# Optimization experiments

Measured on AMD Instinct MI355X. Metric: run time of the kernel, lower is better.

Reference implementation:

```python
import jax, jax.numpy as jnp
import numpy as np

N_WORD, N_DOC, E = 20000, 20000, 500000
H, O, D = 4, 32, 128  # heads, out per head, hidden*heads
NEG_SLOPE = 0.2


def setup_inputs() -> dict:
    key = jax.random.key(0)
    ks = jax.random.split(key, 24)
    rn = lambda k, s, sc=0.1: jax.random.normal(k, s, dtype=jnp.float32) * sc
    ri = lambda k, s, hi: jax.random.randint(k, s, 0, hi, dtype=jnp.int32)
    return {
        'x_word': rn(ks[0], (N_WORD, 300), 1.0),
        'x_doc': rn(ks[1], (N_DOC, D), 1.0),
        'Wp_word': rn(ks[2], (300, D)), 'bp_word': jnp.zeros((D,), jnp.float32),
        'Wp_doc': rn(ks[3], (D, D)), 'bp_doc': jnp.zeros((D,), jnp.float32),
        'Wsrc': rn(ks[4], (2, 3, D, D)), 'bsrc': jnp.zeros((2, 3, D), jnp.float32),
        'Wdst': rn(ks[5], (2, 3, D, D)), 'bdst': jnp.zeros((2, 3, D), jnp.float32),
        'attn': rn(ks[6], (2, 3, H, O)), 'bconv': jnp.zeros((2, 3, D), jnp.float32),
        'Wc1': rn(ks[7], (D, 64)), 'bc1': jnp.zeros((64,), jnp.float32),
        'Wc2': rn(ks[8], (64, 64)), 'bc2': jnp.zeros((64,), jnp.float32),
        'src_wd': ri(ks[9], (E,), N_WORD), 'dst_wd': ri(ks[10], (E,), N_DOC),
        'src_dw': ri(ks[11], (E,), N_DOC), 'dst_dw': ri(ks[12], (E,), N_WORD),
        'src_dd': ri(ks[13], (E,), N_DOC), 'dst_dd': ri(ks[14], (E,), N_DOC),
    }


def _gatv2(h_src, h_dst, src, dst, Ws, bs, Wd, bd, a, bias, n_dst):
    # GATv2Conv (DGL): e = a . leaky_relu(Ws h_u + Wd h_v); edge softmax per dst; sum alpha*Ws h_u
    fs = (h_src @ Ws + bs).reshape(-1, H, O)           # [N_src,H,O]
    fd = (h_dst @ Wd + bd).reshape(-1, H, O)           # [N_dst,H,O]
    e = jax.nn.leaky_relu(fs[src] + fd[dst], NEG_SLOPE)  # [E,H,O]
    score = jnp.einsum('eho,ho->eh', e, a)             # [E,H]
    m = jax.lax.stop_gradient(jax.ops.segment_max(score, dst, num_segments=n_dst))
    ex = jnp.exp(score - m[dst])
    s = jax.ops.segment_sum(ex, dst, num_segments=n_dst)
    alpha = ex / s[dst]                                 # per-dst softmax
    rst = jax.ops.segment_sum(alpha[:, :, None] * fs[src], dst, num_segments=n_dst)
    return rst + bias.reshape(1, H, O)


def reference(x_word, x_doc, Wp_word, bp_word, Wp_doc, bp_doc, Wsrc, bsrc, Wdst, bdst,
              attn, bconv, Wc1, bc1, Wc2, bc2, src_wd, dst_wd, src_dw, dst_dw, src_dd, dst_dd):
    h_w = x_word @ Wp_word + bp_word
    h_d = x_doc @ Wp_doc + bp_doc
    for l in range(2):
        o_wd = _gatv2(h_w, h_d, src_wd, dst_wd, Wsrc[l, 0], bsrc[l, 0], Wdst[l, 0], bdst[l, 0], attn[l, 0], bconv[l, 0], N_DOC)
        o_dw = _gatv2(h_d, h_w, src_dw, dst_dw, Wsrc[l, 1], bsrc[l, 1], Wdst[l, 1], bdst[l, 1], attn[l, 1], bconv[l, 1], N_WORD)
        o_dd = _gatv2(h_d, h_d, src_dd, dst_dd, Wsrc[l, 2], bsrc[l, 2], Wdst[l, 2], bdst[l, 2], attn[l, 2], bconv[l, 2], N_DOC)
        h_d = ((o_wd + o_dd) * 0.5).reshape(N_DOC, D)   # mean over 2 relations into 'document'
        h_w = o_dw.reshape(N_WORD, D)                    # mean over 1 relation into 'word'
    z = jax.nn.relu(h_d @ Wc1 + bc1)
    return z @ Wc2 + bc2  # [N_DOC, len_label]
```

## Files before the change

### kernel.cpp

```cpp
#include <hip/hip_runtime.h>

#define NNODE 20000
#define NEDGE 500000
#define CAP 64
#define RCHUNK 2048
#define NRANGE 8
#define RSZ 2500
#define SCAP 70000
#define XW 64

typedef __attribute__((ext_vector_type(8))) short bf16x8;
typedef __attribute__((ext_vector_type(8))) unsigned short u16x8;
typedef __attribute__((ext_vector_type(4))) float f32x4;

__device__ __forceinline__ unsigned short f2bf(float f) {
    unsigned u = __float_as_uint(f);
    return (unsigned short)((u + 0x7FFFu + ((u >> 16) & 1u)) >> 16);
}
__device__ __forceinline__ float bf2f(unsigned short h) {
    return __uint_as_float((unsigned)h << 16);
}

__device__ __forceinline__ void split_one(
    const float* __restrict__ B, unsigned short* __restrict__ Bt,
    int K, int N, int Kp, int i)
{
    int n = i / Kp, k = i % Kp;
    float v = (k < K) ? B[(size_t)k * N + n] : 0.f;
    unsigned short h = f2bf(v);
    Bt[i] = h;
    Bt[(size_t)N * Kp + i] = f2bf(v - bf2f(h));
}

__device__ __forceinline__ void split_row4(
    const float* __restrict__ X, unsigned short* __restrict__ A2,
    int K, int Kp, int r, int c)
{
    float v[4];
#pragma unroll
    for (int j = 0; j < 4; ++j) v[j] = (c + j < K) ? X[(size_t)r * K + c + j] : 0.f;
    ushort4 hi, lo;
    unsigned short h;
    h = f2bf(v[0]); hi.x = h; lo.x = f2bf(v[0] - bf2f(h));
    h = f2bf(v[1]); hi.y = h; lo.y = f2bf(v[1] - bf2f(h));
    h = f2bf(v[2]); hi.z = h; lo.z = f2bf(v[2] - bf2f(h));
    h = f2bf(v[3]); hi.w = h; lo.w = f2bf(v[3] - bf2f(h));
    *reinterpret_cast<ushort4*>(A2 + (size_t)r * 2 * Kp + c) = hi;
    *reinterpret_cast<ushort4*>(A2 + (size_t)r * 2 * Kp + Kp + c) = lo;
}

__global__ __launch_bounds__(256) void prep_all_kernel(
    const float* __restrict__ Wp_word, const float* __restrict__ Wp_doc,
    const float* __restrict__ Wsrc, const float* __restrict__ Wdst,
    const float* __restrict__ Wc1, const float* __restrict__ Wc2,
    const float* __restrict__ xw, const float* __restrict__ xd,
    unsigned short* __restrict__ WtPw, unsigned short* __restrict__ WtPd,
    unsigned short* __restrict__ WtCat,
    unsigned short* __restrict__ WtC1, unsigned short* __restrict__ WtC2,
    unsigned short* __restrict__ Ax, unsigned short* __restrict__ Axd)
{
    int i = blockIdx.x * 256 + threadIdx.x;
    const int S0 = 128 * 320, S1 = 128 * 128, S2 = 6 * 256 * 128;
    const int S3 = 64 * 128, S4 = 64 * 64;
    const int X1 = NNODE * 80, X2 = NNODE * 32;
    if (i < S0) { split_one(Wp_word, WtPw, 300, 128, 320, i); return; }
    i -= S0;
    if (i < S1) { split_one(Wp_doc, WtPd, 128, 128, 128, i); return; }
    i -= S1;
    if (i < S2) {
        int lc = i / (256 * 128), rem = i % (256 * 128);
        int n = rem / 128, k = rem % 128;
        int l = lc / 3, c = lc % 3;
        int half = n >> 7, nn = n & 127;
        const float* M;
        if (c == 0)      M = half ? (Wdst + (size_t)(l * 3 + 1) * 16384) : (Wsrc + (size_t)(l * 3 + 0) * 16384);
        else if (c == 1) M = half ? (Wsrc + (size_t)(l * 3 + 1) * 16384) : (Wdst + (size_t)(l * 3 + 0) * 16384);
        else             M = half ? (Wdst + (size_t)(l * 3 + 2) * 16384) : (Wsrc + (size_t)(l * 3 + 2) * 16384);
        float v = M[(size_t)k * 128 + nn];
        unsigned short h = f2bf(v);
        unsigned short* Bt = WtCat + (size_t)lc * 65536;
        Bt[(size_t)n * 128 + k] = h;
        Bt[32768 + (size_t)n * 128 + k] = f2bf(v - bf2f(h));
        return;
    }
    i -= S2;
    if (i < S3) { split_one(Wc1, WtC1, 128, 64, 128, i); return; }
    i -= S3;
    if (i < S4) { split_one(Wc2, WtC2, 64, 64, 64, i); return; }
    i -= S4;
    if (i < X1) {
        int r = i / 80, c = (i % 80) * 4;
        split_row4(xw, Ax, 300, 320, r, c);
        return;
    }
    i -= X1;
    if (i < X2) {
        int r = i / 32, c = (i % 32) * 4;
        split_row4(xd, Axd, 128, 128, r, c);
    }
}

template<int BM, int BN, int MODE>
__global__ __launch_bounds__(512) void gemm_mfma_kernel(
    const unsigned short* __restrict__ A2,
    const unsigned short* __restrict__ Bt,
    const float* __restrict__ b0,
    float* __restrict__ C0, unsigned short* __restrict__ S0,
    int M, int Kp, int do_relu)
{
    constexpr int FM = BM / 32;
    constexpr int FN = BN / 64;
    __shared__ unsigned short As[2][BM][40];
    __shared__ unsigned short Bs[2][BN][40];
    const int tid = threadIdx.x;
    const int m0 = blockIdx.x * BM;
    const int wid = tid >> 6, lane = tid & 63;
    const int wm = wid >> 2, wn = wid & 3;
    const int lr = lane & 15, kg = lane >> 4;

    f32x4 acc[FM][FN] = {};
    const size_t KA = 2 * (size_t)Kp;
    const size_t PB = (size_t)BN * Kp;

    for (int k0 = 0; k0 < Kp; k0 += 32) {
#pragma unroll
        for (int idx = tid; idx < BM * 4; idx += 512) {
            int row = idx >> 2, ck = idx & 3;
            u16x8 hi = {0,0,0,0,0,0,0,0}, lo = {0,0,0,0,0,0,0,0};
            if (m0 + row < M) {
                const unsigned short* ap = A2 + (size_t)(m0 + row) * KA + k0 + ck * 8;
                hi = *reinterpret_cast<const u16x8*>(ap);
                lo = *reinterpret_cast<const u16x8*>(ap + Kp);
            }
            *reinterpret_cast<u16x8*>(&As[0][row][ck * 8]) = hi;
            *reinterpret_cast<u16x8*>(&As[1][row][ck * 8]) = lo;
        }
#pragma unroll
        for (int idx = tid; idx < BN * 4; idx += 512) {
            int nr = idx >> 2, ck = idx & 3;
            const unsigned short* bp = Bt + (size_t)nr * Kp + k0 + ck * 8;
            *reinterpret_cast<u16x8*>(&Bs[0][nr][ck * 8]) = *reinterpret_cast<const u16x8*>(bp);
            *reinterpret_cast<u16x8*>(&Bs[1][nr][ck * 8]) = *reinterpret_cast<const u16x8*>(bp + PB);
        }
        __syncthreads();
        bf16x8 ah[FM], al[FM], bh[FN], bl[FN];
#pragma unroll
        for (int fm = 0; fm < FM; ++fm) {
            ah[fm] = *reinterpret_cast<const bf16x8*>(&As[0][wm * (BM / 2) + fm * 16 + lr][kg * 8]);
            al[fm] = *reinterpret_cast<const bf16x8*>(&As[1][wm * (BM / 2) + fm * 16 + lr][kg * 8]);
        }
#pragma unroll
        for (int fn = 0; fn < FN; ++fn) {
            bh[fn] = *reinterpret_cast<const bf16x8*>(&Bs[0][wn * (BN / 4) + fn * 16 + lr][kg * 8]);
            bl[fn] = *reinterpret_cast<const bf16x8*>(&Bs[1][wn * (BN / 4) + fn * 16 + lr][kg * 8]);
        }
#pragma unroll
        for (int fm = 0; fm < FM; ++fm)
#pragma unroll
            for (int fn = 0; fn < FN; ++fn) {
                acc[fm][fn] = __builtin_amdgcn_mfma_f32_16x16x32_bf16(ah[fm], bh[fn], acc[fm][fn], 0, 0, 0);
                acc[fm][fn] = __builtin_amdgcn_mfma_f32_16x16x32_bf16(al[fm], bh[fn], acc[fm][fn], 0, 0, 0);
                acc[fm][fn] = __builtin_amdgcn_mfma_f32_16x16x32_bf16(ah[fm], bl[fn], acc[fm][fn], 0, 0, 0);
            }
        __syncthreads();
    }
#pragma unroll
    for (int fm = 0; fm < FM; ++fm)
#pragma unroll
        for (int fn = 0; fn < FN; ++fn) {
            int gc = wn * (BN / 4) + fn * 16 + lr;
            float bv = b0[gc];
#pragma unroll
            for (int j = 0; j < 4; ++j) {
                int gr = m0 + wm * (BM / 2) + fm * 16 + kg * 4 + j;
                if (gr < M) {
                    float v = acc[fm][fn][j] + bv;
                    if (do_relu) v = fmaxf(v, 0.f);
                    if (MODE == 0) {
                        C0[(size_t)gr * BN + gc] = v;
                    } else {
                        unsigned short h = f2bf(v);
                        S0[(size_t)gr * 2 * BN + gc] = h;
                        S0[(size_t)gr * 2 * BN + BN + gc] = f2bf(v - bf2f(h));
                    }
                }
            }
        }
}

struct Cat3Args {
    const unsigned short* A[3];
    const unsigned short* Bt[3];
    const float* bs0[3];
    const float* bs1[3];
    unsigned short* P0[3];
    unsigned short* P1[3];
};

__global__ __launch_bounds__(512) void gemm_cat3_kernel(Cat3Args args, int M)
{
    constexpr int BM = 128, BN = 256, FM = 4, FN = 4, Kp = 128;
    const int y = blockIdx.y;
    const unsigned short* __restrict__ A2 = args.A[y];
    const unsigned short* __restrict__ Bt = args.Bt[y];
    __shared__ unsigned short As[2][BM][40];
    __shared__ unsigned short Bs[2][BN][40];
    const int tid = threadIdx.x;
    const int m0 = blockIdx.x * BM;
    const int wid = tid >> 6, lane = tid & 63;
    const int wm = wid >> 2, wn = wid & 3;
    const int lr = lane & 15, kg = lane >> 4;

    f32x4 acc[FM][FN] = {};
    const size_t KA = 2 * (size_t)Kp;
    const size_t PB = (size_t)BN * Kp;

    for (int k0 = 0; k0 < Kp; k0 += 32) {
#pragma unroll
        for (int idx = tid; idx < BM * 4; idx += 512) {
            int row = idx >> 2, ck = idx & 3;
            u16x8 hi = {0,0,0,0,0,0,0,0}, lo = {0,0,0,0,0,0,0,0};
            if (m0 + row < M) {
                const unsigned short* ap = A2 + (size_t)(m0 + row) * KA + k0 + ck * 8;
                hi = *reinterpret_cast<const u16x8*>(ap);
                lo = *reinterpret_cast<const u16x8*>(ap + Kp);
            }
            *reinterpret_cast<u16x8*>(&As[0][row][ck * 8]) = hi;
            *reinterpret_cast<u16x8*>(&As[1][row][ck * 8]) = lo;
        }
#pragma unroll
        for (int idx = tid; idx < BN * 4; idx += 512) {
            int nr = idx >> 2, ck = idx & 3;
            const unsigned short* bp = Bt + (size_t)nr * Kp + k0 + ck * 8;
            *reinterpret_cast<u16x8*>(&Bs[0][nr][ck * 8]) = *reinterpret_cast<const u16x8*>(bp);
            *reinterpret_cast<u16x8*>(&Bs[1][nr][ck * 8]) = *reinterpret_cast<const u16x8*>(bp + PB);
        }
        __syncthreads();
        bf16x8 ah[FM], al[FM], bh[FN], bl[FN];
#pragma unroll
        for (int fm = 0; fm < FM; ++fm) {
            ah[fm] = *reinterpret_cast<const bf16x8*>(&As[0][wm * 64 + fm * 16 + lr][kg * 8]);
            al[fm] = *reinterpret_cast<const bf16x8*>(&As[1][wm * 64 + fm * 16 + lr][kg * 8]);
        }
#pragma unroll
        for (int fn = 0; fn < FN; ++fn) {
            bh[fn] = *reinterpret_cast<const bf16x8*>(&Bs[0][wn * 64 + fn * 16 + lr][kg * 8]);
            bl[fn] = *reinterpret_cast<const bf16x8*>(&Bs[1][wn * 64 + fn * 16 + lr][kg * 8]);
        }
#pragma unroll
        for (int fm = 0; fm < FM; ++fm)
#pragma unroll
            for (int fn = 0; fn < FN; ++fn) {
                acc[fm][fn] = __builtin_amdgcn_mfma_f32_16x16x32_bf16(ah[fm], bh[fn], acc[fm][fn], 0, 0, 0);
                acc[fm][fn] = __builtin_amdgcn_mfma_f32_16x16x32_bf16(al[fm], bh[fn], acc[fm][fn], 0, 0, 0);
                acc[fm][fn] = __builtin_amdgcn_mfma_f32_16x16x32_bf16(ah[fm], bl[fn], acc[fm][fn], 0, 0, 0);
            }
        __syncthreads();
    }
    const float* __restrict__ bs0 = args.bs0[y];
    const float* __restrict__ bs1 = args.bs1[y];
    unsigned short* __restrict__ P0 = args.P0[y];
    unsigned short* __restrict__ P1 = args.P1[y];
#pragma unroll
    for (int fm = 0; fm < FM; ++fm)
#pragma unroll
        for (int fn = 0; fn < FN; ++fn) {
            int gc = wn * 64 + fn * 16 + lr;
            float bv = (gc < 128) ? bs0[gc] : bs1[gc - 128];
#pragma unroll
            for (int j = 0; j < 4; ++j) {
                int gr = m0 + wm * 64 + fm * 16 + kg * 4 + j;
                if (gr < M) {
                    float v = acc[fm][fn][j] + bv;
                    unsigned short h = f2bf(v);
                    if (gc < 128) P0[(size_t)gr * 128 + gc] = h;
                    else          P1[(size_t)gr * 128 + gc - 128] = h;
                }
            }
        }
}

__global__ __launch_bounds__(256) void route_kernel(
    const int* __restrict__ s0, const int* __restrict__ d0,
    const int* __restrict__ s1, const int* __restrict__ d1,
    const int* __restrict__ s2, const int* __restrict__ d2,
    unsigned* __restrict__ stage, int* __restrict__ scur)
{
    __shared__ unsigned sbuf[RCHUNK];
    __shared__ int hcnt[NRANGE], hoff[NRANGE], gbase[NRANGE], hcur[NRANGE];
    const int rel = blockIdx.y;
    const int c0 = blockIdx.x * RCHUNK;
    const int n = (c0 + RCHUNK <= NEDGE) ? RCHUNK : (NEDGE - c0);
    const int tid = threadIdx.x;
    const int* sp = rel == 0 ? s0 : rel == 1 ? s1 : s2;
    const int* dp = rel == 0 ? d0 : rel == 1 ? d1 : d2;

    if (tid < NRANGE) hcnt[tid] = 0;
    __syncthreads();
    for (int i = tid; i < n; i += 256) atomicAdd(&hcnt[dp[c0 + i] / RSZ], 1);
    __syncthreads();
    if (tid == 0) {
        int o = 0;
        for (int r = 0; r < NRANGE; ++r) {
            hoff[r] = o; hcur[r] = o; o += hcnt[r];
            gbase[r] = atomicAdd(&scur[rel * NRANGE + r], hcnt[r]);
        }
    }
    __syncthreads();
    for (int i = tid; i < n; i += 256) {
        int d = dp[c0 + i], s = sp[c0 + i];
        int k = atomicAdd(&hcur[d / RSZ], 1);
        sbuf[k] = ((unsigned)d << 16) | (unsigned)s;
    }
    __syncthreads();
    for (int r = 0; r < NRANGE; ++r) {
        int cnt = hcnt[r];
        int lim = SCAP - gbase[r];
        if (cnt > lim) cnt = lim;
        unsigned* dst = stage + (size_t)(rel * NRANGE + r) * SCAP + gbase[r];
        for (int i = tid; i < cnt; i += 256) dst[i] = sbuf[hoff[r] + i];
    }
}

__global__ __launch_bounds__(256) void xfill_kernel(
    const unsigned* __restrict__ stage, const int* __restrict__ scur,
    int* __restrict__ deg, unsigned short* __restrict__ csr)
{
    const int r = blockIdx.x & 7;
    const int w = blockIdx.x >> 3;
    const int tid = threadIdx.x;
#pragma unroll
    for (int rel = 0; rel < 3; ++rel) {
        int total = scur[rel * NRANGE + r];
        if (total > SCAP) total = SCAP;
        const unsigned* st = stage + (size_t)(rel * NRANGE + r) * SCAP;
        int* dg = deg + rel * NNODE;
        unsigned short* cb = csr + (size_t)rel * NNODE * CAP;
        for (int i = w * 256 + tid; i < total; i += XW * 256) {
            unsigned p = st[i];
            int d = (int)(p >> 16), s = (int)(p & 0xFFFFu);
            int k = atomicAdd(&dg[d], 1);
            if (k < CAP) cb[(size_t)d * CAP + k] = (unsigned short)s;
        }
    }
}

__device__ __forceinline__ void rel_raw(
    const unsigned short* __restrict__ fsP,
    const unsigned short* __restrict__ fdP,
    const unsigned short* __restrict__ csrc,
    const float* __restrict__ attnRow,
    int d, int lane, int iBeg, int iEnd,
    float& ssum, float* __restrict__ acc)
{
    float fdv[8], av[8];
    {
        u16x8 t = *reinterpret_cast<const u16x8*>(fdP + (size_t)d * 128 + lane * 8);
#pragma unroll
        for (int j = 0; j < 8; ++j) fdv[j] = bf2f(t[j]);
    }
#pragma unroll
    for (int j = 0; j < 8; ++j) av[j] = attnRow[lane * 8 + j];

    int i = iBeg;
    for (; i + 4 <= iEnd; i += 4) {
        int s0 = csrc[i], s1 = csrc[i + 1], s2 = csrc[i + 2], s3 = csrc[i + 3];
        u16x8 q0 = *reinterpret_cast<const u16x8*>(fsP + (size_t)s0 * 128 + lane * 8);
        u16x8 q1 = *reinterpret_cast<const u16x8*>(fsP + (size_t)s1 * 128 + lane * 8);
        u16x8 q2 = *reinterpret_cast<const u16x8*>(fsP + (size_t)s2 * 128 + lane * 8);
        u16x8 q3 = *reinterpret_cast<const u16x8*>(fsP + (size_t)s3 * 128 + lane * 8);
        float u0[8], u1[8], u2[8], u3[8];
        float pa0 = 0.f, pb0 = 0.f, pa1 = 0.f, pb1 = 0.f;
        float pa2 = 0.f, pb2 = 0.f, pa3 = 0.f, pb3 = 0.f;
#pragma unroll
        for (int j = 0; j < 8; ++j) {
            u0[j] = bf2f(q0[j]); float z = u0[j] + fdv[j];
            pa0 = fmaf(av[j], z, pa0); pb0 = fmaf(av[j], fabsf(z), pb0);
        }
#pragma unroll
        for (int j = 0; j < 8; ++j) {
            u1[j] = bf2f(q1[j]); float z = u1[j] + fdv[j];
            pa1 = fmaf(av[j], z, pa1); pb1 = fmaf(av[j], fabsf(z), pb1);
        }
#pragma unroll
        for (int j = 0; j < 8; ++j) {
            u2[j] = bf2f(q2[j]); float z = u2[j] + fdv[j];
            pa2 = fmaf(av[j], z, pa2); pb2 = fmaf(av[j], fabsf(z), pb2);
        }
#pragma unroll
        for (int j = 0; j < 8; ++j) {
            u3[j] = bf2f(q3[j]); float z = u3[j] + fdv[j];
            pa3 = fmaf(av[j], z, pa3); pb3 = fmaf(av[j], fabsf(z), pb3);
        }
        float p0 = fmaf(0.4f, pb0, 0.6f * pa0);
        float p1 = fmaf(0.4f, pb1, 0.6f * pa1);
        float p2 = fmaf(0.4f, pb2, 0.6f * pa2);
        float p3 = fmaf(0.4f, pb3, 0.6f * pa3);
        p0 += __shfl_xor(p0, 1); p0 += __shfl_xor(p0, 2);
        p1 += __shfl_xor(p1, 1); p1 += __shfl_xor(p1, 2);
        p2 += __shfl_xor(p2, 1); p2 += __shfl_xor(p2, 2);
        p3 += __shfl_xor(p3, 1); p3 += __shfl_xor(p3, 2);
        float w0 = __expf(p0), w1 = __expf(p1);
        float w2 = __expf(p2), w3 = __expf(p3);
        ssum += (w0 + w1) + (w2 + w3);
#pragma unroll
        for (int j = 0; j < 8; ++j)
            acc[j] += fmaf(w0, u0[j], w1 * u1[j]) + fmaf(w2, u2[j], w3 * u3[j]);
    }
    for (; i < iEnd; ++i) {
        int s0 = csrc[i];
        u16x8 q0 = *reinterpret_cast<const u16x8*>(fsP + (size_t)s0 * 128 + lane * 8);
        float u0[8];
        float pa = 0.f, pb = 0.f;
#pragma unroll
        for (int j = 0; j < 8; ++j) {
            u0[j] = bf2f(q0[j]); float z = u0[j] + fdv[j];
            pa = fmaf(av[j], z, pa); pb = fmaf(av[j], fabsf(z), pb);
        }
        float p0 = fmaf(0.4f, pb, 0.6f * pa);
        p0 += __shfl_xor(p0, 1); p0 += __shfl_xor(p0, 2);
        float w = __expf(p0);
        ssum += w;
#pragma unroll
        for (int j = 0; j < 8; ++j) acc[j] = fmaf(w, u0[j], acc[j]);
    }
}

struct ConvJob {
    const unsigned short *fsA, *fdA;
    const int* degA; const unsigned short* csrA;
    const float *attnA, *biasA;
    const unsigned short *fsB, *fdB;
    const int* degB; const unsigned short* csrB;
    const float *attnB, *biasB;
    float wscale;
    unsigned short* sp;
};

__global__ __launch_bounds__(256) void gat_conv3_kernel(
    ConvJob J0, ConvJob J1, int nblk0)
{
    const bool first = ((int)blockIdx.x < nblk0);
    const ConvJob J = first ? J0 : J1;
    const int b = first ? (int)blockIdx.x : (int)blockIdx.x - nblk0;
    int gid = b * 256 + threadIdx.x;
    int d = gid >> 5;
    int lane = gid & 15;
    int half = (gid >> 4) & 1;
    if (d >= NNODE) return;

    float ssum = 0.f;
    float acc[8];
#pragma unroll
    for (int j = 0; j < 8; ++j) acc[j] = 0.f;
    float r[8];

    if (J.fsB) {
        const unsigned short* fs = half ? J.fsB : J.fsA;
        const unsigned short* fd = half ? J.fdB : J.fdA;
        const int* dgp           = half ? J.degB : J.degA;
        const unsigned short* cs = half ? J.csrB : J.csrA;
        const float* at          = half ? J.attnB : J.attnA;
        int deg = dgp[d]; if (deg > CAP) deg = CAP;
        rel_raw(fs, fd, cs, at, d, lane, d * CAP, d * CAP + deg, ssum, acc);
        float inv = (ssum > 0.f) ? J.wscale / ssum : 0.f;
#pragma unroll
        for (int j = 0; j < 8; ++j) {
            r[j] = inv * acc[j];
            r[j] += __shfl_xor(r[j], 16);
        }
    } else {
        int deg = J.degA[d]; if (deg > CAP) deg = CAP;
        int h = (deg + 1) >> 1;
        int iB = d * CAP + (half ? h : 0);
        int iE = d * CAP + (half ? deg : h);
        rel_raw(J.fsA, J.fdA, J.csrA, J.attnA, d, lane, iB, iE, ssum, acc);
        ssum += __shfl_xor(ssum, 16);
#pragma unroll
        for (int j = 0; j < 8; ++j) acc[j] += __shfl_xor(acc[j], 16);
        float inv = (ssum > 0.f) ? J.wscale / ssum : 0.f;
#pragma unroll
        for (int j = 0; j < 8; ++j) r[j] = inv * acc[j];
    }

    if (half == 0) {
        u16x8 hv, lv;
#pragma unroll
        for (int j = 0; j < 8; ++j) {
            float bb = J.biasA[lane * 8 + j];
            if (J.biasB) bb += J.biasB[lane * 8 + j];
            float o = J.wscale * bb + r[j];
            unsigned short hh = f2bf(o);
            hv[j] = hh;
            lv[j] = f2bf(o - bf2f(hh));
        }
        *reinterpret_cast<u16x8*>(J.sp + (size_t)d * 256 + lane * 8) = hv;
        *reinterpret_cast<u16x8*>(J.sp + (size_t)d * 256 + 128 + lane * 8) = lv;
    }
}

extern "C" void kernel_launch(void* const* d_in, const int* in_sizes, int n_in,
                              void* d_out, int out_size, void* d_ws, size_t ws_size,
                              hipStream_t stream)
{
    const float* x_word  = (const float*)d_in[0];
    const float* x_doc   = (const float*)d_in[1];
    const float* Wp_word = (const float*)d_in[2];
    const float* bp_word = (const float*)d_in[3];
    const float* Wp_doc  = (const float*)d_in[4];
    const float* bp_doc  = (const float*)d_in[5];
    const float* Wsrc    = (const float*)d_in[6];
    const float* bsrc    = (const float*)d_in[7];
    const float* Wdst    = (const float*)d_in[8];
    const float* bdst    = (const float*)d_in[9];
    const float* attn    = (const float*)d_in[10];
    const float* bconv   = (const float*)d_in[11];
    const float* Wc1     = (const float*)d_in[12];
    const float* bc1     = (const float*)d_in[13];
    const float* Wc2     = (const float*)d_in[14];
    const float* bc2     = (const float*)d_in[15];
    const int* src_wd = (const int*)d_in[16];
    const int* dst_wd = (const int*)d_in[17];
    const int* src_dw = (const int*)d_in[18];
    const int* dst_dw = (const int*)d_in[19];
    const int* src_dd = (const int*)d_in[20];
    const int* dst_dd = (const int*)d_in[21];

    const size_t NP = (size_t)NNODE * 128;
    unsigned short* U = (unsigned short*)d_ws;
    unsigned short* Pfs_wd = U;
    unsigned short* Pfd_dw = U + 1 * NP;
    unsigned short* Pfd_wd = U + 2 * NP;
    unsigned short* Pfs_dw = U + 3 * NP;
    unsigned short* Pfs_dd = U + 4 * NP;
    unsigned short* Pfd_dd = U + 5 * NP;
    unsigned short* AswA = U + 6 * NP;
    unsigned short* AsdA = AswA + 2 * NP;
    unsigned short* AswB = AsdA + 2 * NP;
    unsigned short* AsdB = AswB + 2 * NP;
    unsigned short* WtPw  = AsdB + 2 * NP;
    unsigned short* WtPd  = WtPw + 81920;
    unsigned short* WtCat = WtPd + 32768;
    unsigned short* WtC1  = WtCat + 393216;
    unsigned short* WtC2  = WtC1 + 16384;
    unsigned short* Ax  = Pfs_wd;
    unsigned short* Axd = AswB;
    unsigned short* Az  = AswB;
    int* I    = (int*)(WtC2 + 8192);
    int* deg  = I;
    int* scur = I + 3 * NNODE;
    unsigned* stage = (unsigned*)(scur + 32);
    unsigned short* csrp = (unsigned short*)(stage + 3 * NRANGE * SCAP);

    const int GB128 = (NNODE + 127) / 128;
    const int CB32 = (NNODE * 32) / 256;
    const int RB = (NEDGE + RCHUNK - 1) / RCHUNK;

    (void)hipMemsetAsync(deg, 0, (3 * NNODE + 32) * sizeof(int), stream);
    route_kernel<<<dim3(RB, 3), 256, 0, stream>>>(
        src_wd, dst_wd, src_dw, dst_dw, src_dd, dst_dd, stage, scur);
    xfill_kernel<<<NRANGE * XW, 256, 0, stream>>>(stage, scur, deg, csrp);

    const int PREP = 266240 + NNODE * 112;
    prep_all_kernel<<<(PREP + 255) / 256, 256, 0, stream>>>(
        Wp_word, Wp_doc, Wsrc, Wdst, Wc1, Wc2, x_word, x_doc,
        WtPw, WtPd, WtCat, WtC1, WtC2, Ax, Axd);

    gemm_mfma_kernel<128, 128, 2><<<GB128, 512, 0, stream>>>(
        Ax, WtPw, bp_word, nullptr, AswA, NNODE, 320, 0);
    gemm_mfma_kernel<128, 128, 2><<<GB128, 512, 0, stream>>>(
        Axd, WtPd, bp_doc, nullptr, AsdA, NNODE, 128, 0);

    const unsigned short* Asw_in = AswA;
    const unsigned short* Asd_in = AsdA;
    for (int l = 0; l < 2; ++l) {
        const int l3 = l * 3;
        Cat3Args ca;
        ca.A[0] = Asw_in; ca.A[1] = Asd_in; ca.A[2] = Asd_in;
        ca.Bt[0] = WtCat + (size_t)(l3 + 0) * 65536;
        ca.Bt[1] = WtCat + (size_t)(l3 + 1) * 65536;
        ca.Bt[2] = WtCat + (size_t)(l3 + 2) * 65536;
        ca.bs0[0] = bsrc + (l3 + 0) * 128; ca.bs1[0] = bdst + (l3 + 1) * 128;
        ca.bs0[1] = bdst + (l3 + 0) * 128; ca.bs1[1] = bsrc + (l3 + 1) * 128;
        ca.bs0[2] = bsrc + (l3 + 2) * 128; ca.bs1[2] = bdst + (l3 + 2) * 128;
        ca.P0[0] = Pfs_wd; ca.P1[0] = Pfd_dw;
        ca.P0[1] = Pfd_wd; ca.P1[1] = Pfs_dw;
        ca.P0[2] = Pfs_dd; ca.P1[2] = Pfd_dd;
        gemm_cat3_kernel<<<dim3(GB128, 3), 512, 0, stream>>>(ca, NNODE);

        ConvJob jd;
        jd.fsA = Pfs_wd; jd.fdA = Pfd_wd; jd.degA = deg;             jd.csrA = csrp;
        jd.attnA = attn + (l3 + 0) * 128; jd.biasA = bconv + (l3 + 0) * 128;
        jd.fsB = Pfs_dd; jd.fdB = Pfd_dd; jd.degB = deg + 2 * NNODE; jd.csrB = csrp + (size_t)2 * NNODE * CAP;
        jd.attnB = attn + (l3 + 2) * 128; jd.biasB = bconv + (l3 + 2) * 128;
        jd.wscale = 0.5f; jd.sp = (l == 0 ? AsdB : AsdA);

        if (l == 0) {
            ConvJob jw;
            jw.fsA = Pfs_dw; jw.fdA = Pfd_dw; jw.degA = deg + NNODE; jw.csrA = csrp + (size_t)NNODE * CAP;
            jw.attnA = attn + (l3 + 1) * 128; jw.biasA = bconv + (l3 + 1) * 128;
            jw.fsB = nullptr; jw.fdB = nullptr; jw.degB = nullptr; jw.csrB = nullptr;
            jw.attnB = nullptr; jw.biasB = nullptr;
            jw.wscale = 1.0f; jw.sp = AswB;
            gat_conv3_kernel<<<2 * CB32, 256, 0, stream>>>(jd, jw, CB32);
        } else {
            gat_conv3_kernel<<<CB32, 256, 0, stream>>>(jd, jd, CB32);
        }
        Asw_in = AswB;
        Asd_in = AsdB;
    }

    gemm_mfma_kernel<128, 64, 2><<<GB128, 512, 0, stream>>>(
        AsdA, WtC1, bc1, nullptr, Az, NNODE, 128, 1);
    gemm_mfma_kernel<128, 64, 0><<<GB128, 512, 0, stream>>>(
        Az, WtC2, bc2, (float*)d_out, nullptr, NNODE, 64, 0);
}
```

Measured before the change: 370.6 us.

## Fuse routing with weight prep, batch projection GEMMs, widen GAT conv to 64 lanes per node

Merges the edge-routing kernel into the weight/input split kernel as extra blocks, and launches both input projection GEMMs in one grid via a shared gemm body. The GAT aggregation kernel now assigns 64 threads per destination node instead of 32, splitting each node's edge list into two or four segments and combining them with extra cross-lane shuffles. The goal is fewer launches and more parallelism per high-degree node. The cost is more shuffle reductions and shared-memory use in the fused prep kernel.

```diff
diff --git a/kernel.cpp b/kernel.cpp
--- a/kernel.cpp
+++ b/kernel.cpp
@@ -49,7 +49,13 @@
     *reinterpret_cast<ushort4*>(A2 + (size_t)r * 2 * Kp + Kp + c) = lo;
 }
 
-__global__ __launch_bounds__(256) void prep_all_kernel(
+#define RB_ROUTE ((NEDGE + RCHUNK - 1) / RCHUNK)
+
+__global__ __launch_bounds__(256) void build_prep_kernel(
+    const int* __restrict__ s0, const int* __restrict__ d0,
+    const int* __restrict__ s1, const int* __restrict__ d1,
+    const int* __restrict__ s2, const int* __restrict__ d2,
+    unsigned* __restrict__ stage, int* __restrict__ scur,
     const float* __restrict__ Wp_word, const float* __restrict__ Wp_doc,
     const float* __restrict__ Wsrc, const float* __restrict__ Wdst,
     const float* __restrict__ Wc1, const float* __restrict__ Wc2,
@@ -59,7 +65,44 @@
     unsigned short* __restrict__ WtC1, unsigned short* __restrict__ WtC2,
     unsigned short* __restrict__ Ax, unsigned short* __restrict__ Axd)
 {
-    int i = blockIdx.x * 256 + threadIdx.x;
+    __shared__ unsigned sbuf[RCHUNK];
+    __shared__ int hcnt[NRANGE], hoff[NRANGE], gbase[NRANGE], hcur[NRANGE];
+    const int tid = threadIdx.x;
+    if ((int)blockIdx.x < 3 * RB_ROUTE) {
+        const int rel = blockIdx.x / RB_ROUTE;
+        const int c0 = (blockIdx.x % RB_ROUTE) * RCHUNK;
+        const int n = (c0 + RCHUNK <= NEDGE) ? RCHUNK : (NEDGE - c0);
+        const int* sp = rel == 0 ? s0 : rel == 1 ? s1 : s2;
+        const int* dp = rel == 0 ? d0 : rel == 1 ? d1 : d2;
+
+        if (tid < NRANGE) hcnt[tid] = 0;
+        __syncthreads();
+        for (int i = tid; i < n; i += 256) atomicAdd(&hcnt[dp[c0 + i] / RSZ], 1);
+        __syncthreads();
+        if (tid == 0) {
+            int o = 0;
+            for (int r = 0; r < NRANGE; ++r) {
+                hoff[r] = o; hcur[r] = o; o += hcnt[r];
+                gbase[r] = atomicAdd(&scur[rel * NRANGE + r], hcnt[r]);
+            }
+        }
+        __syncthreads();
+        for (int i = tid; i < n; i += 256) {
+            int d = dp[c0 + i], s = sp[c0 + i];
+            int k = atomicAdd(&hcur[d / RSZ], 1);
+            sbuf[k] = ((unsigned)d << 16) | (unsigned)s;
+        }
+        __syncthreads();
+        for (int r = 0; r < NRANGE; ++r) {
+            int cnt = hcnt[r];
+            int lim = SCAP - gbase[r];
+            if (cnt > lim) cnt = lim;
+            unsigned* dst = stage + (size_t)(rel * NRANGE + r) * SCAP + gbase[r];
+            for (int i = tid; i < cnt; i += 256) dst[i] = sbuf[hoff[r] + i];
+        }
+        return;
+    }
+    int i = ((int)blockIdx.x - 3 * RB_ROUTE) * 256 + tid;
     const int S0 = 128 * 320, S1 = 128 * 128, S2 = 6 * 256 * 128;
     const int S3 = 64 * 128, S4 = 64 * 64;
     const int X1 = NNODE * 80, X2 = NNODE * 32;
@@ -100,20 +143,41 @@
     }
 }
 
+__global__ __launch_bounds__(256) void xfill_kernel(
+    const unsigned* __restrict__ stage, const int* __restrict__ scur,
+    int* __restrict__ deg, unsigned short* __restrict__ csr)
+{
+    const int r = blockIdx.x & 7;
+    const int w = blockIdx.x >> 3;
+    const int tid = threadIdx.x;
+#pragma unroll
+    for (int rel = 0; rel < 3; ++rel) {
+        int total = scur[rel * NRANGE + r];
+        if (total > SCAP) total = SCAP;
+        const unsigned* st = stage + (size_t)(rel * NRANGE + r) * SCAP;
+        int* dg = deg + rel * NNODE;
+        unsigned short* cb = csr + (size_t)rel * NNODE * CAP;
+        for (int i = w * 256 + tid; i < total; i += XW * 256) {
+            unsigned p = st[i];
+            int d = (int)(p >> 16), s = (int)(p & 0xFFFFu);
+            int k = atomicAdd(&dg[d], 1);
+            if (k < CAP) cb[(size_t)d * CAP + k] = (unsigned short)s;
+        }
+    }
+}
+
 template<int BM, int BN, int MODE>
-__global__ __launch_bounds__(512) void gemm_mfma_kernel(
+__device__ __forceinline__ void gemm_body(
     const unsigned short* __restrict__ A2,
     const unsigned short* __restrict__ Bt,
     const float* __restrict__ b0,
     float* __restrict__ C0, unsigned short* __restrict__ S0,
-    int M, int Kp, int do_relu)
+    int M, int Kp, int do_relu, int m0,
+    unsigned short (*As)[BM][40], unsigned short (*Bs)[BN][40])
 {
     constexpr int FM = BM / 32;
     constexpr int FN = BN / 64;
-    __shared__ unsigned short As[2][BM][40];
-    __shared__ unsigned short Bs[2][BN][40];
     const int tid = threadIdx.x;
-    const int m0 = blockIdx.x * BM;
     const int wid = tid >> 6, lane = tid & 63;
     const int wm = wid >> 2, wn = wid & 3;
     const int lr = lane & 15, kg = lane >> 4;
@@ -188,6 +252,37 @@
         }
 }
 
+template<int BM, int BN, int MODE>
+__global__ __launch_bounds__(512) void gemm_mfma_kernel(
+    const unsigned short* __restrict__ A2,
+    const unsigned short* __restrict__ Bt,
+    const float* __restrict__ b0,
+    float* __restrict__ C0, unsigned short* __restrict__ S0,
+    int M, int Kp, int do_relu)
+{
+    __shared__ unsigned short As[2][BM][40];
+    __shared__ unsigned short Bs[2][BN][40];
+    gemm_body<BM, BN, MODE>(A2, Bt, b0, C0, S0, M, Kp, do_relu,
+                            blockIdx.x * BM, As, Bs);
+}
+
+struct Proj2Args {
+    const unsigned short* A[2];
+    const unsigned short* Bt[2];
+    const float* b0[2];
+    unsigned short* S0[2];
+    int Kp[2];
+};
+
+__global__ __launch_bounds__(512) void gemm_proj2_kernel(Proj2Args a, int M)
+{
+    __shared__ unsigned short As[2][128][40];
+    __shared__ unsigned short Bs[2][128][40];
+    const int y = blockIdx.y;
+    gemm_body<128, 128, 2>(a.A[y], a.Bt[y], a.b0[y], nullptr, a.S0[y],
+                           M, a.Kp[y], 0, blockIdx.x * 128, As, Bs);
+}
+
 struct Cat3Args {
     const unsigned short* A[3];
     const unsigned short* Bt[3];
@@ -280,71 +375,6 @@
         }
 }
 
-__global__ __launch_bounds__(256) void route_kernel(
-    const int* __restrict__ s0, const int* __restrict__ d0,
-    const int* __restrict__ s1, const int* __restrict__ d1,
-    const int* __restrict__ s2, const int* __restrict__ d2,
-    unsigned* __restrict__ stage, int* __restrict__ scur)
-{
-    __shared__ unsigned sbuf[RCHUNK];
-    __shared__ int hcnt[NRANGE], hoff[NRANGE], gbase[NRANGE], hcur[NRANGE];
-    const int rel = blockIdx.y;
-    const int c0 = blockIdx.x * RCHUNK;
-    const int n = (c0 + RCHUNK <= NEDGE) ? RCHUNK : (NEDGE - c0);
-    const int tid = threadIdx.x;
-    const int* sp = rel == 0 ? s0 : rel == 1 ? s1 : s2;
-    const int* dp = rel == 0 ? d0 : rel == 1 ? d1 : d2;
-
-    if (tid < NRANGE) hcnt[tid] = 0;
-    __syncthreads();
-    for (int i = tid; i < n; i += 256) atomicAdd(&hcnt[dp[c0 + i] / RSZ], 1);
-    __syncthreads();
-    if (tid == 0) {
-        int o = 0;
-        for (int r = 0; r < NRANGE; ++r) {
-            hoff[r] = o; hcur[r] = o; o += hcnt[r];
-            gbase[r] = atomicAdd(&scur[rel * NRANGE + r], hcnt[r]);
-        }
-    }
-    __syncthreads();
-    for (int i = tid; i < n; i += 256) {
-        int d = dp[c0 + i], s = sp[c0 + i];
-        int k = atomicAdd(&hcur[d / RSZ], 1);
-        sbuf[k] = ((unsigned)d << 16) | (unsigned)s;
-    }
-    __syncthreads();
-    for (int r = 0; r < NRANGE; ++r) {
-        int cnt = hcnt[r];
-        int lim = SCAP - gbase[r];
-        if (cnt > lim) cnt = lim;
-        unsigned* dst = stage + (size_t)(rel * NRANGE + r) * SCAP + gbase[r];
-        for (int i = tid; i < cnt; i += 256) dst[i] = sbuf[hoff[r] + i];
-    }
-}
-
-__global__ __launch_bounds__(256) void xfill_kernel(
-    const unsigned* __restrict__ stage, const int* __restrict__ scur,
-    int* __restrict__ deg, unsigned short* __restrict__ csr)
-{
-    const int r = blockIdx.x & 7;
-    const int w = blockIdx.x >> 3;
-    const int tid = threadIdx.x;
-#pragma unroll
-    for (int rel = 0; rel < 3; ++rel) {
-        int total = scur[rel * NRANGE + r];
-        if (total > SCAP) total = SCAP;
-        const unsigned* st = stage + (size_t)(rel * NRANGE + r) * SCAP;
-        int* dg = deg + rel * NNODE;
-        unsigned short* cb = csr + (size_t)rel * NNODE * CAP;
-        for (int i = w * 256 + tid; i < total; i += XW * 256) {
-            unsigned p = st[i];
-            int d = (int)(p >> 16), s = (int)(p & 0xFFFFu);
-            int k = atomicAdd(&dg[d], 1);
-            if (k < CAP) cb[(size_t)d * CAP + k] = (unsigned short)s;
-        }
-    }
-}
-
 __device__ __forceinline__ void rel_raw(
     const unsigned short* __restrict__ fsP,
     const unsigned short* __restrict__ fdP,
@@ -437,16 +467,16 @@
     unsigned short* sp;
 };
 
-__global__ __launch_bounds__(256) void gat_conv3_kernel(
+__global__ __launch_bounds__(256) void gat_conv4_kernel(
     ConvJob J0, ConvJob J1, int nblk0)
 {
     const bool first = ((int)blockIdx.x < nblk0);
     const ConvJob J = first ? J0 : J1;
     const int b = first ? (int)blockIdx.x : (int)blockIdx.x - nblk0;
-    int gid = b * 256 + threadIdx.x;
-    int d = gid >> 5;
-    int lane = gid & 15;
-    int half = (gid >> 4) & 1;
+    const int tid = threadIdx.x;
+    const int d = b * 4 + (tid >> 6);
+    const int lane = tid & 15;
+    const int group = (tid >> 4) & 3;
     if (d >= NNODE) return;
 
     float ssum = 0.f;
@@ -456,34 +486,44 @@
     float r[8];
 
     if (J.fsB) {
-        const unsigned short* fs = half ? J.fsB : J.fsA;
-        const unsigned short* fd = half ? J.fdB : J.fdA;
-        const int* dgp           = half ? J.degB : J.degA;
-        const unsigned short* cs = half ? J.csrB : J.csrA;
-        const float* at          = half ? J.attnB : J.attnA;
+        const int rel = group >> 1, hf = group & 1;
+        const unsigned short* fs = rel ? J.fsB : J.fsA;
+        const unsigned short* fd = rel ? J.fdB : J.fdA;
+        const int* dgp           = rel ? J.degB : J.degA;
+        const unsigned short* cs = rel ? J.csrB : J.csrA;
+        const float* at          = rel ? J.attnB : J.attnA;
         int deg = dgp[d]; if (deg > CAP) deg = CAP;
-        rel_raw(fs, fd, cs, at, d, lane, d * CAP, d * CAP + deg, ssum, acc);
+        int h0 = (deg + 1) >> 1;
+        int iB = d * CAP + (hf ? h0 : 0);
+        int iE = d * CAP + (hf ? deg : h0);
+        rel_raw(fs, fd, cs, at, d, lane, iB, iE, ssum, acc);
+        ssum += __shfl_xor(ssum, 16);
+#pragma unroll
+        for (int j = 0; j < 8; ++j) acc[j] += __shfl_xor(acc[j], 16);
         float inv = (ssum > 0.f) ? J.wscale / ssum : 0.f;
 #pragma unroll
         for (int j = 0; j < 8; ++j) {
             r[j] = inv * acc[j];
-            r[j] += __shfl_xor(r[j], 16);
+            r[j] += __shfl_xor(r[j], 32);
         }
     } else {
         int deg = J.degA[d]; if (deg > CAP) deg = CAP;
-        int h = (deg + 1) >> 1;
-        int iB = d * CAP + (half ? h : 0);
-        int iE = d * CAP + (half ? deg : h);
+        int iB = d * CAP + ((deg * group) >> 2);
+        int iE = d * CAP + ((deg * (group + 1)) >> 2);
         rel_raw(J.fsA, J.fdA, J.csrA, J.attnA, d, lane, iB, iE, ssum, acc);
         ssum += __shfl_xor(ssum, 16);
-#pragma unroll
-        for (int j = 0; j < 8; ++j) acc[j] += __shfl_xor(acc[j], 16);
+        ssum += __shfl_xor(ssum, 32);
+#pragma unroll
+        for (int j = 0; j < 8; ++j) {
+            acc[j] += __shfl_xor(acc[j], 16);
+            acc[j] += __shfl_xor(acc[j], 32);
+        }
         float inv = (ssum > 0.f) ? J.wscale / ssum : 0.f;
 #pragma unroll
         for (int j = 0; j < 8; ++j) r[j] = inv * acc[j];
     }
 
-    if (half == 0) {
+    if (group == 0) {
         u16x8 hv, lv;
 #pragma unroll
         for (int j = 0; j < 8; ++j) {
@@ -553,23 +593,21 @@
     unsigned short* csrp = (unsigned short*)(stage + 3 * NRANGE * SCAP);
 
     const int GB128 = (NNODE + 127) / 128;
-    const int CB32 = (NNODE * 32) / 256;
-    const int RB = (NEDGE + RCHUNK - 1) / RCHUNK;
+    const int CB4 = (NNODE + 3) / 4;
+    const int PREP = 266240 + NNODE * 112;
+    const int BPB = 3 * RB_ROUTE + (PREP + 255) / 256;
 
     (void)hipMemsetAsync(deg, 0, (3 * NNODE + 32) * sizeof(int), stream);
-    route_kernel<<<dim3(RB, 3), 256, 0, stream>>>(
-        src_wd, dst_wd, src_dw, dst_dw, src_dd, dst_dd, stage, scur);
-    xfill_kernel<<<NRANGE * XW, 256, 0, stream>>>(stage, scur, deg, csrp);
-
-    const int PREP = 266240 + NNODE * 112;
-    prep_all_kernel<<<(PREP + 255) / 256, 256, 0, stream>>>(
+    build_prep_kernel<<<BPB, 256, 0, stream>>>(
+        src_wd, dst_wd, src_dw, dst_dw, src_dd, dst_dd, stage, scur,
         Wp_word, Wp_doc, Wsrc, Wdst, Wc1, Wc2, x_word, x_doc,
         WtPw, WtPd, WtCat, WtC1, WtC2, Ax, Axd);
-
-    gemm_mfma_kernel<128, 128, 2><<<GB128, 512, 0, stream>>>(
-        Ax, WtPw, bp_word, nullptr, AswA, NNODE, 320, 0);
-    gemm_mfma_kernel<128, 128, 2><<<GB128, 512, 0, stream>>>(
-        Axd, WtPd, bp_doc, nullptr, AsdA, NNODE, 128, 0);
+    xfill_kernel<<<NRANGE * XW, 256, 0, stream>>>(stage, scur, deg, csrp);
+
+    Proj2Args pa;
+    pa.A[0] = Ax;  pa.Bt[0] = WtPw; pa.b0[0] = bp_word; pa.S0[0] = AswA; pa.Kp[0] = 320;
+    pa.A[1] = Axd; pa.Bt[1] = WtPd; pa.b0[1] = bp_doc;  pa.S0[1] = AsdA; pa.Kp[1] = 128;
+    gemm_proj2_kernel<<<dim3(GB128, 2), 512, 0, stream>>>(pa, NNODE);
 
     const unsigned short* Asw_in = AswA;
     const unsigned short* Asd_in = AsdA;
@@ -602,9 +640,9 @@
             jw.fsB = nullptr; jw.fdB = nullptr; jw.degB = nullptr; jw.csrB = nullptr;
             jw.attnB = nullptr; jw.biasB = nullptr;
             jw.wscale = 1.0f; jw.sp = AswB;
-            gat_conv3_kernel<<<2 * CB32, 256, 0, stream>>>(jd, jw, CB32);
+            gat_conv4_kernel<<<2 * CB4, 256, 0, stream>>>(jd, jw, CB4);
         } else {
-            gat_conv3_kernel<<<CB32, 256, 0, stream>>>(jd, jd, CB32);
+            gat_conv4_kernel<<<CB4, 256, 0, stream>>>(jd, jd, CB4);
         }
         Asw_in = AswB;
         Asd_in = AsdB;
```

After: 369.5 us. No clear change (-0.3%).
